# Kernel optimization log

Measured on AMD Instinct MI355X. Metric: run time of the kernel, lower is better.

Reference implementation:

```python
import jax, jax.numpy as jnp
import numpy as np

POOL = 2  # pool_size from init_kwargs


def setup_inputs() -> dict:
    key = jax.random.key(0)
    b, n = 8192, 64
    A = jax.random.normal(key, (b, n, n), dtype=jnp.float32)
    # SPD construction: A A^T / n + I  (well-conditioned, distinct eigvals a.s.)
    X = A @ jnp.swapaxes(A, -1, -2) / n + jnp.eye(n, dtype=jnp.float32)
    return {"X": X}


def _logm_spd(X):
    # matrix log of batched SPD via eigendecomposition (SPDTangentSpace)
    w, V = jnp.linalg.eigh(X)
    return (V * jnp.log(w)[..., None, :]) @ jnp.swapaxes(V, -1, -2)


def _expm_sym(H):
    # matrix exp of batched symmetric matrices (SPDUnTangentSpace)
    w, V = jnp.linalg.eigh(H)
    return (V * jnp.exp(w)[..., None, :]) @ jnp.swapaxes(V, -1, -2)


def reference(X):
    # log map to tangent space
    logX = _logm_spd(X)
    b, n, _ = logX.shape
    m = n // POOL
    # avg_pool2d(kernel=POOL, stride=POOL) over the (n, n) matrix dims
    pooled = logX.reshape(b, m, POOL, m, POOL).mean(axis=(2, 4))
    # pooling of a symmetric matrix with this block pattern stays symmetric;
    # symmetrize for numerical safety before eigh-based exp map
    pooled = 0.5 * (pooled + jnp.swapaxes(pooled, -1, -2))
    return _expm_sym(pooled)
```

## Files before the change

kernel.cpp:

```cpp
#include <hip/hip_runtime.h>

typedef __attribute__((ext_vector_type(8))) short short8;
typedef __attribute__((ext_vector_type(16))) float f32x16;

#define PL 8256
#define SLOT 16448
#define U0O 0
#define U1O SLOT
#define U2O (2 * SLOT)

__device__ __forceinline__ int swadr(int m, int kc) {
  return m * 128 + ((kc ^ (m & 7)) << 4);
}

__device__ __forceinline__ unsigned int cvtpk(float a, float b) {
  unsigned int r;
  asm("v_cvt_pk_bf16_f32 %0, %1, %2" : "=v"(r) : "v"(a), "v"(b));
  return r;
}

__device__ __forceinline__ float dppswap(float v) {
  return __int_as_float(
      __builtin_amdgcn_mov_dpp(__float_as_int(v), 0xB1, 0xF, 0xF, true));
}

__device__ __forceinline__ f32x16 zero16() {
  f32x16 z;
#pragma unroll
  for (int i = 0; i < 16; ++i) z[i] = 0.f;
  return z;
}

__device__ __forceinline__ void q16x16(f32x16& v) {
#pragma unroll
  for (int r = 0; r < 16; r += 2) {
    unsigned w = cvtpk(v[r], v[r + 1]);
    v[r] = __uint_as_float(w << 16);
    v[r + 1] = __uint_as_float(w & 0xFFFF0000u);
  }
}

__device__ __forceinline__ void store_hi8(char* dst, const float* v) {
  uint4 w = make_uint4(cvtpk(v[0], v[1]), cvtpk(v[2], v[3]),
                       cvtpk(v[4], v[5]), cvtpk(v[6], v[7]));
  *(uint4*)dst = w;
}

__device__ __forceinline__ void split_store8(char* dst, const float* v) {
  unsigned h[4], l[4];
#pragma unroll
  for (int j = 0; j < 4; ++j) {
    unsigned hw = cvtpk(v[2 * j], v[2 * j + 1]);
    float h0 = __uint_as_float(hw << 16);
    float h1 = __uint_as_float(hw & 0xFFFF0000u);
    l[j] = cvtpk(v[2 * j] - h0, v[2 * j + 1] - h1);
    h[j] = hw;
  }
  *(uint4*)dst = make_uint4(h[0], h[1], h[2], h[3]);
  *(uint4*)(dst + PL) = make_uint4(l[0], l[1], l[2], l[3]);
}

__device__ __forceinline__ void split_store4(char* dst, const float* v) {
  unsigned h0 = cvtpk(v[0], v[1]), h1 = cvtpk(v[2], v[3]);
  unsigned l0 = cvtpk(v[0] - __uint_as_float(h0 << 16),
                      v[1] - __uint_as_float(h0 & 0xFFFF0000u));
  unsigned l1 = cvtpk(v[2] - __uint_as_float(h1 << 16),
                      v[3] - __uint_as_float(h1 & 0xFFFF0000u));
  *(uint2*)dst = make_uint2(h0, h1);
  *(uint2*)(dst + PL) = make_uint2(l0, l1);
}

template <int NK, int OA, int OB>
__device__ __forceinline__ void mac1(f32x16& acc, char* const (&pA)[4],
                                     char* const (&pB)[4]) {
#pragma unroll
  for (int s = 0; s < NK; ++s) {
    short8 a = *(const short8*)(pA[s] + OA);
    short8 b = *(const short8*)(pB[s] + OB);
    acc = __builtin_amdgcn_mfma_f32_32x32x16_bf16(a, b, acc, 0, 0, 0);
  }
}

template <int NK, int OA, int OB>
__device__ __forceinline__ void mac2A(f32x16& acc, char* const (&pA)[4],
                                      char* const (&pB)[4]) {
#pragma unroll
  for (int s = 0; s < NK; ++s) {
    short8 ah = *(const short8*)(pA[s] + OA);
    short8 al = *(const short8*)(pA[s] + OA + PL);
    short8 b = *(const short8*)(pB[s] + OB);
    acc = __builtin_amdgcn_mfma_f32_32x32x16_bf16(ah, b, acc, 0, 0, 0);
    acc = __builtin_amdgcn_mfma_f32_32x32x16_bf16(al, b, acc, 0, 0, 0);
  }
}

template <int NK, int OA, int OB>
__device__ __forceinline__ void mac2B(f32x16& acc, char* const (&pA)[4],
                                      char* const (&pB)[4]) {
#pragma unroll
  for (int s = 0; s < NK; ++s) {
    short8 a = *(const short8*)(pA[s] + OA);
    short8 bh = *(const short8*)(pB[s] + OB);
    short8 bl = *(const short8*)(pB[s] + OB + PL);
    acc = __builtin_amdgcn_mfma_f32_32x32x16_bf16(a, bh, acc, 0, 0, 0);
    acc = __builtin_amdgcn_mfma_f32_32x32x16_bf16(a, bl, acc, 0, 0, 0);
  }
}

template <int NK, int OA, int OB>
__device__ __forceinline__ void mac3(f32x16& acc, char* const (&pA)[4],
                                     char* const (&pB)[4]) {
#pragma unroll
  for (int s = 0; s < NK; ++s) {
    short8 ah = *(const short8*)(pA[s] + OA);
    short8 al = *(const short8*)(pA[s] + OA + PL);
    short8 bh = *(const short8*)(pB[s] + OB);
    short8 bl = *(const short8*)(pB[s] + OB + PL);
    acc = __builtin_amdgcn_mfma_f32_32x32x16_bf16(ah, bh, acc, 0, 0, 0);
    acc = __builtin_amdgcn_mfma_f32_32x32x16_bf16(ah, bl, acc, 0, 0, 0);
    acc = __builtin_amdgcn_mfma_f32_32x32x16_bf16(al, bh, acc, 0, 0, 0);
  }
}

template <int OFF>
__device__ __forceinline__ void write_hi(char* lds, const int (&wo)[16], bool ev,
                                         const f32x16& vals) {
#pragma unroll
  for (int r = 0; r < 16; ++r) {
    float vn = dppswap(vals[r]);
    unsigned hw = cvtpk(vals[r], vn);
    if (ev) *(unsigned*)(lds + OFF + wo[r]) = hw;
  }
}

template <int OFF>
__device__ __forceinline__ void write_split(char* lds, const int (&wo)[16],
                                            bool ev, int pl, const f32x16& vals,
                                            int r0, int r1) {
#pragma unroll
  for (int r = 0; r < 16; ++r) {
    if (r < r0 || r >= r1) continue;
    float v = vals[r];
    float vn = dppswap(v);
    unsigned hw = cvtpk(v, vn);
    float lo = v - __uint_as_float(hw << 16);
    float lon = dppswap(lo);
    unsigned lw = cvtpk(lon, lo);
    *(unsigned*)(lds + OFF + pl + wo[r]) = ev ? hw : lw;
  }
}

__global__ void __launch_bounds__(256, 3)
spd_pool_kernel(const float* __restrict__ X, float* __restrict__ out) {
  __shared__ __align__(16) char lds[3 * SLOT];

  const int tid = threadIdx.x;
  const int lane = tid & 63;
  const int wv = tid >> 6;
  const int R = (wv >> 1) * 32;
  const int Cc = (wv & 1) * 32;
  const int half = lane >> 5;
  const int ln31 = lane & 31;
  const bool ev = (ln31 & 1) == 0;
  const int pl = ev ? 0 : PL;

  char* pA[4];
  char* pB[4];
#pragma unroll
  for (int s = 0; s < 4; ++s) {
    const int kc = 2 * s + half;
    pA[s] = lds + swadr(R + ln31, kc);
    pB[s] = lds + swadr(Cc + ln31, kc);
  }

  int wo[16];
  {
    const int col0 = Cc + (ln31 & ~1);
    const int cchunk = col0 >> 3, cbyte = (col0 & 7) * 2;
    const int rbase = R + 4 * half;
#pragma unroll
    for (int r = 0; r < 16; ++r) {
      const int m = rbase + (r & 3) + 8 * (r >> 2);
      wo[r] = m * 128 + ((cchunk ^ (m & 7)) << 4) + cbyte;
    }
  }

  f32x16 dmask;
#pragma unroll
  for (int r = 0; r < 16; ++r)
    dmask[r] = (R + (r & 3) + 8 * (r >> 2) + 4 * half == Cc + ln31) ? 1.f : 0.f;

  f32x16 mY, mZ;

  {
    const int em = tid >> 2;
    const int ekc = (tid & 3) * 2;
    const int ec0 = ekc * 8;
    const float ic1 = 1.0f / 6.6f;
    const float* Xg = X + (size_t)blockIdx.x * 4096 + em * 64 + ec0;
    const float4* xp = (const float4*)Xg;
    float4 a = xp[0], b = xp[1], c = xp[2], d = xp[3];
    float v[16] = {a.x * ic1, a.y * ic1, a.z * ic1, a.w * ic1,
                   b.x * ic1, b.y * ic1, b.z * ic1, b.w * ic1,
                   c.x * ic1, c.y * ic1, c.z * ic1, c.w * ic1,
                   d.x * ic1, d.y * ic1, d.z * ic1, d.w * ic1};
    float t[16];
#pragma unroll
    for (int i = 0; i < 16; ++i)
      t[i] = ((em == ec0 + i) ? 1.5f : 0.f) - 0.5f * v[i];
    split_store8(lds + swadr(em, ekc), v);
    split_store8(lds + swadr(em, ekc + 1), v + 8);
    store_hi8(lds + U1O + swadr(em, ekc), t);
    store_hi8(lds + U1O + swadr(em, ekc + 1), t + 8);
  }
  __syncthreads();
  mY = zero16();
  mac1<4, U0O, U1O>(mY, pA, pB);
  write_hi<U2O>(lds, wo, ev, mY);
  __syncthreads();
#pragma unroll 1
  for (int it = 0; it < 4; ++it) {
    f32x16 a;
#pragma unroll
    for (int r = 0; r < 16; ++r) a[r] = -3.f * dmask[r];
    mac1<4, U1O, U2O>(a, pA, pB);
    f32x16 tv;
#pragma unroll
    for (int r = 0; r < 16; ++r) tv[r] = -0.5f * a[r];
    write_hi<U2O + PL>(lds, wo, ev, tv);
    __syncthreads();
    mY = zero16();
    mac1<4, U2O, U2O + PL>(mY, pA, pB);
    mZ = zero16();
    mac1<4, U2O + PL, U1O>(mZ, pA, pB);
    __syncthreads();
    write_hi<U2O>(lds, wo, ev, mY);
    write_hi<U1O>(lds, wo, ev, mZ);
    __syncthreads();
  }
  mY = zero16();
  mac2A<4, U0O, U1O>(mY, pA, pB);
  write_split<U2O>(lds, wo, ev, pl, mY, 0, 16);
  __syncthreads();
  {
    f32x16 a;
#pragma unroll
    for (int r = 0; r < 16; ++r) a[r] = -dmask[r];
    mac2B<4, U1O, U2O>(a, pA, pB);
    f32x16 dv;
#pragma unroll
    for (int r = 0; r < 16; ++r) dv[r] = -0.5f * a[r];
    write_hi<U0O>(lds, wo, ev, dv);
  }
  __syncthreads();
  mac1<4, U2O, U0O>(mY, pA, pB);
  __syncthreads();
  write_split<U2O>(lds, wo, ev, pl, mY, 0, 16);
  {
    f32x16 t0v;
#pragma unroll
    for (int r = 0; r < 16; ++r) t0v[r] = 1.5f * dmask[r] - 0.5f * mY[r];
    write_hi<U1O>(lds, wo, ev, t0v);
  }
  __syncthreads();
  mY = zero16();
  mac1<4, U2O, U1O>(mY, pA, pB);
  write_hi<U0O>(lds, wo, ev, mY);
  __syncthreads();
#pragma unroll 1
  for (int it = 0; it < 2; ++it) {
    f32x16 a;
#pragma unroll
    for (int r = 0; r < 16; ++r) a[r] = -3.f * dmask[r];
    mac1<4, U1O, U0O>(a, pA, pB);
    f32x16 tv;
#pragma unroll
    for (int r = 0; r < 16; ++r) tv[r] = -0.5f * a[r];
    write_hi<U0O + PL>(lds, wo, ev, tv);
    __syncthreads();
    mY = zero16();
    mac1<4, U0O, U0O + PL>(mY, pA, pB);
    mZ = zero16();
    mac1<4, U0O + PL, U1O>(mZ, pA, pB);
    __syncthreads();
    write_hi<U0O>(lds, wo, ev, mY);
    write_hi<U1O>(lds, wo, ev, mZ);
    __syncthreads();
  }
  q16x16(mZ);
  mY = zero16();
  mac2A<4, U2O, U1O>(mY, pA, pB);
  write_split<U0O>(lds, wo, ev, pl, mY, 0, 16);
  __syncthreads();
  {
    f32x16 a;
#pragma unroll
    for (int r = 0; r < 16; ++r) a[r] = -dmask[r];
    mac2B<4, U1O, U0O>(a, pA, pB);
    f32x16 dv;
#pragma unroll
    for (int r = 0; r < 16; ++r) dv[r] = -0.5f * a[r];
    write_hi<U2O>(lds, wo, ev, dv);
  }
  __syncthreads();
  mac1<4, U0O, U2O>(mY, pA, pB);
  mac1<4, U2O, U1O>(mZ, pA, pB);
  __syncthreads();
  write_split<U0O>(lds, wo, ev, pl, mY, 0, 16);
  q16x16(mZ);
  write_hi<U1O>(lds, wo, ev, mZ);
  __syncthreads();
  {
    f32x16 a;
#pragma unroll
    for (int r = 0; r < 16; ++r) a[r] = -dmask[r];
    mac2B<4, U1O, U0O>(a, pA, pB);
    f32x16 dv;
#pragma unroll
    for (int r = 0; r < 16; ++r) dv[r] = -0.5f * a[r];
    write_hi<U2O>(lds, wo, ev, dv);
  }
  __syncthreads();
  mac1<4, U0O, U2O>(mY, pA, pB);
  mac1<4, U2O, U1O>(mZ, pA, pB);
  f32x16 sv;
  {
    const float ca = 0.80141224f;
    const float cb = 0.31194493f;
#pragma unroll
    for (int r = 0; r < 16; ++r) sv[r] = ca * mY[r] - cb * mZ[r];
  }
  __syncthreads();
  write_split<U0O>(lds, wo, ev, pl, sv, 0, 16);
  __syncthreads();
  {
    f32x16 s2 = zero16();
    mac3<4, U0O, U0O>(s2, pA, pB);
    const float A11 = -0.08948864f, A9 = 0.12152778f;
    f32x16 qv;
#pragma unroll
    for (int r = 0; r < 16; ++r) qv[r] = A11 * s2[r] + A9 * dmask[r];
    write_hi<U1O>(lds, wo, ev, s2);
    write_hi<U1O + PL>(lds, wo, ev, qv);
  }
  __syncthreads();
  {
    const float acoef[3] = {-0.17857143f, 0.3f, -0.66666667f};
#pragma unroll 1
    for (int j = 0; j < 3; ++j) {
      f32x16 a;
#pragma unroll
      for (int r = 0; r < 16; ++r) a[r] = acoef[j] * dmask[r];
      mac1<4, U1O + PL, U1O>(a, pA, pB);
      __syncthreads();
      write_hi<U1O + PL>(lds, wo, ev, a);
      __syncthreads();
    }
  }
  {
    f32x16 a;
#pragma unroll
    for (int r = 0; r < 16; ++r) a[r] = 4.f * dmask[r];
    mac1<4, U1O + PL, U1O>(a, pA, pB);
    __syncthreads();
    write_split<U2O>(lds, wo, ev, pl, a, 0, 16);
    __syncthreads();
  }
  {
    f32x16 mL = zero16();
    mac3<4, U0O, U2O>(mL, pA, pB);
    float* Lf = (float*)(lds + U1O);
#pragma unroll
    for (int r = 0; r < 16; ++r)
      Lf[(R + (r & 3) + 8 * (r >> 2) + 4 * half) * 64 + Cc + ln31] = mL[r];
  }
  __syncthreads();
  {
    const float d8 = 2.4801587e-5f, d7 = 1.9841270e-4f;
    const float* Lf = (const float*)(lds + U1O);
    int i = tid >> 3, ct = tid & 7, j4 = ct * 4;
    const float4* r0p = (const float4*)&Lf[(2 * i) * 64 + 8 * ct];
    const float4* r1p = (const float4*)&Lf[(2 * i + 1) * 64 + 8 * ct];
    float4 a0 = r0p[0], a1 = r0p[1], b0 = r1p[0], b1 = r1p[1];
    float p[4], q2v[4];
    p[0] = 0.125f * (a0.x + a0.y + b0.x + b0.y);
    p[1] = 0.125f * (a0.z + a0.w + b0.z + b0.w);
    p[2] = 0.125f * (a1.x + a1.y + b1.x + b1.y);
    p[3] = 0.125f * (a1.z + a1.w + b1.z + b1.w);
#pragma unroll
    for (int qq = 0; qq < 4; ++qq)
      q2v[qq] = d8 * p[qq] + ((i == j4 + qq) ? d7 : 0.f);
    int boff = swadr(i, ct >> 1) + (j4 & 7) * 2;
    split_store4(lds + boff, p);
    split_store4(lds + U2O + boff, q2v);
  }
  __syncthreads();
  char* pE[4];
#pragma unroll
  for (int s = 0; s < 4; ++s) pE[s] = lds + swadr(ln31, 2 * s + half);
  f32x16 dmask2;
#pragma unroll
  for (int r = 0; r < 16; ++r)
    dmask2[r] = ((r & 3) + 8 * (r >> 2) + 4 * half == ln31) ? 1.f : 0.f;
  int wo2[16];
  {
    const int col0 = ln31 & ~1;
    const int cchunk = col0 >> 3, cbyte = (col0 & 7) * 2;
    const int rbase = 4 * half;
#pragma unroll
    for (int r = 0; r < 16; ++r) {
      const int m = rbase + (r & 3) + 8 * (r >> 2);
      wo2[r] = m * 128 + ((cchunk ^ (m & 7)) << 4) + cbyte;
    }
  }
  {
    const float dcoef[7] = {1.f / 720.f, 1.f / 120.f, 1.f / 24.f,
                            1.f / 6.f,   0.5f,        1.f,       1.f};
#pragma unroll 1
    for (int j = 0; j < 7; ++j) {
      f32x16 acc;
#pragma unroll
      for (int r = 0; r < 16; ++r) acc[r] = dcoef[j] * dmask2[r];
      mac3<2, U2O, U0O>(acc, pE, pE);
      __syncthreads();
      write_split<U2O>(lds, wo2, ev, pl, acc, 4 * wv, 4 * wv + 4);
      __syncthreads();
    }
  }
  {
    f32x16 acc = zero16();
    mac3<2, U2O, U2O>(acc, pE, pE);
    float* og = out + (size_t)blockIdx.x * 1024;
#pragma unroll
    for (int r = 0; r < 16; ++r) {
      if (r < 4 * wv || r >= 4 * wv + 4) continue;
      int rl = (r & 3) + 8 * (r >> 2) + 4 * half;
      og[rl * 32 + ln31] = acc[r];
    }
  }
}

extern "C" void kernel_launch(void* const* d_in, const int* in_sizes, int n_in,
                              void* d_out, int out_size, void* d_ws, size_t ws_size,
                              hipStream_t stream) {
  const float* X = (const float*)d_in[0];
  float* out = (float*)d_out;
  const int batch = in_sizes[0] / 4096;
  spd_pool_kernel<<<batch, 256, 0, stream>>>(X, out);
}
```

Baseline: 541.5 us.

## Process each matrix with a single wavefront, removing block barriers

Changes the kernel from four waves per 64x64 matrix, each computing one 32x32 tile, to one 64-lane wave computing all four tiles in registers. This removes every __syncthreads and the cross-wave LDS handoffs, and avg-pooling is now done in registers with DPP instead of through an fp32 LDS staging buffer. LDS is repacked into five 8 KB planes. In exchange each wave does four times the MFMA work serially and holds many more accumulator registers. Per-CU occupancy and latency hiding now depend on how many single-wave blocks can be resident at once.

```diff
diff --git a/kernel.cpp b/kernel.cpp
--- a/kernel.cpp
+++ b/kernel.cpp
@@ -3,35 +3,91 @@
 typedef __attribute__((ext_vector_type(8))) short short8;
 typedef __attribute__((ext_vector_type(16))) float f32x16;
 
-#define PL 8256
-#define SLOT 16448
-#define U0O 0
-#define U1O SLOT
-#define U2O (2 * SLOT)
+#define PP0 0
+#define PP1 8192
+#define PP2 16384
+#define PP3 24576
+#define PP4 32768
+
+#define MFMA32(a, b, c) __builtin_amdgcn_mfma_f32_32x32x16_bf16((a), (b), (c), 0, 0, 0)
 
 __device__ __forceinline__ int swadr(int m, int kc) {
   return m * 128 + ((kc ^ (m & 7)) << 4);
 }
-
-__device__ __forceinline__ unsigned int cvtpk(float a, float b) {
-  unsigned int r;
+__device__ __forceinline__ unsigned cvtpk(float a, float b) {
+  unsigned r;
   asm("v_cvt_pk_bf16_f32 %0, %1, %2" : "=v"(r) : "v"(a), "v"(b));
   return r;
 }
-
 __device__ __forceinline__ float dppswap(float v) {
   return __int_as_float(
       __builtin_amdgcn_mov_dpp(__float_as_int(v), 0xB1, 0xF, 0xF, true));
 }
-
-__device__ __forceinline__ f32x16 zero16() {
-  f32x16 z;
-#pragma unroll
-  for (int i = 0; i < 16; ++i) z[i] = 0.f;
-  return z;
-}
-
-__device__ __forceinline__ void q16x16(f32x16& v) {
+__device__ __forceinline__ short8 ldf(const char* p, int off) {
+  return *(const short8*)(p + off);
+}
+
+template <int OA, int OB, bool SA, bool SB>
+__device__ __forceinline__ void mm64(f32x16& C0, f32x16& C1, f32x16& C2, f32x16& C3,
+                                     const char* lds, const int (&pk)[4]) {
+#pragma unroll
+  for (int s = 0; s < 4; ++s) {
+    short8 a0 = ldf(lds, pk[s] + OA);
+    short8 a1 = ldf(lds, pk[s] + OA + 4096);
+    short8 b0 = ldf(lds, pk[s] + OB);
+    short8 b1 = ldf(lds, pk[s] + OB + 4096);
+    C0 = MFMA32(a0, b0, C0);
+    C1 = MFMA32(a0, b1, C1);
+    C2 = MFMA32(a1, b0, C2);
+    C3 = MFMA32(a1, b1, C3);
+    if constexpr (SB) {
+      short8 b0l = ldf(lds, pk[s] + OB + 8192);
+      short8 b1l = ldf(lds, pk[s] + OB + 8192 + 4096);
+      C0 = MFMA32(a0, b0l, C0);
+      C1 = MFMA32(a0, b1l, C1);
+      C2 = MFMA32(a1, b0l, C2);
+      C3 = MFMA32(a1, b1l, C3);
+    }
+    if constexpr (SA) {
+      short8 a0l = ldf(lds, pk[s] + OA + 8192);
+      short8 a1l = ldf(lds, pk[s] + OA + 8192 + 4096);
+      C0 = MFMA32(a0l, b0, C0);
+      C1 = MFMA32(a0l, b1, C1);
+      C2 = MFMA32(a1l, b0, C2);
+      C3 = MFMA32(a1l, b1, C3);
+    }
+  }
+}
+
+template <int OA, int OB>
+__device__ __forceinline__ void mm32(f32x16& C, const char* lds, const int (&pk)[4]) {
+#pragma unroll
+  for (int s = 0; s < 2; ++s) {
+    short8 ah = ldf(lds, pk[s] + OA);
+    short8 al = ldf(lds, pk[s] + OA + 8192);
+    short8 bh = ldf(lds, pk[s] + OB);
+    short8 bl = ldf(lds, pk[s] + OB + 8192);
+    C = MFMA32(ah, bh, C);
+    C = MFMA32(ah, bl, C);
+    C = MFMA32(al, bh, C);
+  }
+}
+
+__device__ __forceinline__ void z4(f32x16& C0, f32x16& C1, f32x16& C2, f32x16& C3) {
+#pragma unroll
+  for (int r = 0; r < 16; ++r) {
+    C0[r] = 0.f; C1[r] = 0.f; C2[r] = 0.f; C3[r] = 0.f;
+  }
+}
+__device__ __forceinline__ void pre4(f32x16& C0, f32x16& C1, f32x16& C2, f32x16& C3,
+                                     const f32x16& dm, float v) {
+#pragma unroll
+  for (int r = 0; r < 16; ++r) {
+    float d = v * dm[r];
+    C0[r] = d; C3[r] = d; C1[r] = 0.f; C2[r] = 0.f;
+  }
+}
+__device__ __forceinline__ void q16t(f32x16& v) {
 #pragma unroll
   for (int r = 0; r < 16; r += 2) {
     unsigned w = cvtpk(v[r], v[r + 1]);
@@ -40,379 +96,252 @@
   }
 }
 
-__device__ __forceinline__ void store_hi8(char* dst, const float* v) {
-  uint4 w = make_uint4(cvtpk(v[0], v[1]), cvtpk(v[2], v[3]),
-                       cvtpk(v[4], v[5]), cvtpk(v[6], v[7]));
-  *(uint4*)dst = w;
-}
-
-__device__ __forceinline__ void split_store8(char* dst, const float* v) {
-  unsigned h[4], l[4];
-#pragma unroll
-  for (int j = 0; j < 4; ++j) {
-    unsigned hw = cvtpk(v[2 * j], v[2 * j + 1]);
-    float h0 = __uint_as_float(hw << 16);
-    float h1 = __uint_as_float(hw & 0xFFFF0000u);
-    l[j] = cvtpk(v[2 * j] - h0, v[2 * j + 1] - h1);
-    h[j] = hw;
-  }
-  *(uint4*)dst = make_uint4(h[0], h[1], h[2], h[3]);
-  *(uint4*)(dst + PL) = make_uint4(l[0], l[1], l[2], l[3]);
-}
-
-__device__ __forceinline__ void split_store4(char* dst, const float* v) {
-  unsigned h0 = cvtpk(v[0], v[1]), h1 = cvtpk(v[2], v[3]);
-  unsigned l0 = cvtpk(v[0] - __uint_as_float(h0 << 16),
-                      v[1] - __uint_as_float(h0 & 0xFFFF0000u));
-  unsigned l1 = cvtpk(v[2] - __uint_as_float(h1 << 16),
-                      v[3] - __uint_as_float(h1 & 0xFFFF0000u));
-  *(uint2*)dst = make_uint2(h0, h1);
-  *(uint2*)(dst + PL) = make_uint2(l0, l1);
-}
-
-template <int NK, int OA, int OB>
-__device__ __forceinline__ void mac1(f32x16& acc, char* const (&pA)[4],
-                                     char* const (&pB)[4]) {
-#pragma unroll
-  for (int s = 0; s < NK; ++s) {
-    short8 a = *(const short8*)(pA[s] + OA);
-    short8 b = *(const short8*)(pB[s] + OB);
-    acc = __builtin_amdgcn_mfma_f32_32x32x16_bf16(a, b, acc, 0, 0, 0);
-  }
-}
-
-template <int NK, int OA, int OB>
-__device__ __forceinline__ void mac2A(f32x16& acc, char* const (&pA)[4],
-                                      char* const (&pB)[4]) {
-#pragma unroll
-  for (int s = 0; s < NK; ++s) {
-    short8 ah = *(const short8*)(pA[s] + OA);
-    short8 al = *(const short8*)(pA[s] + OA + PL);
-    short8 b = *(const short8*)(pB[s] + OB);
-    acc = __builtin_amdgcn_mfma_f32_32x32x16_bf16(ah, b, acc, 0, 0, 0);
-    acc = __builtin_amdgcn_mfma_f32_32x32x16_bf16(al, b, acc, 0, 0, 0);
-  }
-}
-
-template <int NK, int OA, int OB>
-__device__ __forceinline__ void mac2B(f32x16& acc, char* const (&pA)[4],
-                                      char* const (&pB)[4]) {
-#pragma unroll
-  for (int s = 0; s < NK; ++s) {
-    short8 a = *(const short8*)(pA[s] + OA);
-    short8 bh = *(const short8*)(pB[s] + OB);
-    short8 bl = *(const short8*)(pB[s] + OB + PL);
-    acc = __builtin_amdgcn_mfma_f32_32x32x16_bf16(a, bh, acc, 0, 0, 0);
-    acc = __builtin_amdgcn_mfma_f32_32x32x16_bf16(a, bl, acc, 0, 0, 0);
-  }
-}
-
-template <int NK, int OA, int OB>
-__device__ __forceinline__ void mac3(f32x16& acc, char* const (&pA)[4],
-                                     char* const (&pB)[4]) {
-#pragma unroll
-  for (int s = 0; s < NK; ++s) {
-    short8 ah = *(const short8*)(pA[s] + OA);
-    short8 al = *(const short8*)(pA[s] + OA + PL);
-    short8 bh = *(const short8*)(pB[s] + OB);
-    short8 bl = *(const short8*)(pB[s] + OB + PL);
-    acc = __builtin_amdgcn_mfma_f32_32x32x16_bf16(ah, bh, acc, 0, 0, 0);
-    acc = __builtin_amdgcn_mfma_f32_32x32x16_bf16(ah, bl, acc, 0, 0, 0);
-    acc = __builtin_amdgcn_mfma_f32_32x32x16_bf16(al, bh, acc, 0, 0, 0);
+template <int OFF, bool SCALE, bool ADDI>
+__device__ __forceinline__ void wrhi64(char* lds, const int (&wo)[16], bool ev, int jd,
+                                       const f32x16& C0, const f32x16& C1,
+                                       const f32x16& C2, const f32x16& C3,
+                                       const f32x16& dm, float al, float be) {
+#pragma unroll
+  for (int t = 0; t < 4; ++t) {
+    const f32x16& C = t == 0 ? C0 : t == 1 ? C1 : t == 2 ? C2 : C3;
+    const int base = OFF + (t >> 1) * 4096 + ((t & 1) ? jd : 0);
+#pragma unroll
+    for (int r = 0; r < 16; ++r) {
+      float v = SCALE ? al * C[r] : C[r];
+      if (ADDI && (t == 0 || t == 3)) v += be * dm[r];
+      float vn = dppswap(v);
+      unsigned hw = cvtpk(v, vn);
+      if (ev) *(unsigned*)(lds + base + wo[r]) = hw;
+    }
   }
 }
 
 template <int OFF>
-__device__ __forceinline__ void write_hi(char* lds, const int (&wo)[16], bool ev,
-                                         const f32x16& vals) {
+__device__ __forceinline__ void wrsp64(char* lds, const int (&wo)[16], bool ev, int pl,
+                                       int jd, const f32x16& C0, const f32x16& C1,
+                                       const f32x16& C2, const f32x16& C3) {
+#pragma unroll
+  for (int t = 0; t < 4; ++t) {
+    const f32x16& C = t == 0 ? C0 : t == 1 ? C1 : t == 2 ? C2 : C3;
+    const int base = OFF + (t >> 1) * 4096 + ((t & 1) ? jd : 0) + pl;
+#pragma unroll
+    for (int r = 0; r < 16; ++r) {
+      float v = C[r];
+      float vn = dppswap(v);
+      unsigned hw = cvtpk(v, vn);
+      float lo = v - __uint_as_float(hw << 16);
+      float lon = dppswap(lo);
+      unsigned lw = cvtpk(lon, lo);
+      *(unsigned*)(lds + base + wo[r]) = ev ? hw : lw;
+    }
+  }
+}
+
+template <int OFF>
+__device__ __forceinline__ void wrsp32(char* lds, const int (&wo)[16], bool ev, int pl,
+                                       const f32x16& C) {
+  const int base = OFF + pl;
 #pragma unroll
   for (int r = 0; r < 16; ++r) {
-    float vn = dppswap(vals[r]);
-    unsigned hw = cvtpk(vals[r], vn);
-    if (ev) *(unsigned*)(lds + OFF + wo[r]) = hw;
-  }
-}
-
-template <int OFF>
-__device__ __forceinline__ void write_split(char* lds, const int (&wo)[16],
-                                            bool ev, int pl, const f32x16& vals,
-                                            int r0, int r1) {
-#pragma unroll
-  for (int r = 0; r < 16; ++r) {
-    if (r < r0 || r >= r1) continue;
-    float v = vals[r];
+    float v = C[r];
     float vn = dppswap(v);
     unsigned hw = cvtpk(v, vn);
     float lo = v - __uint_as_float(hw << 16);
     float lon = dppswap(lo);
     unsigned lw = cvtpk(lon, lo);
-    *(unsigned*)(lds + OFF + pl + wo[r]) = ev ? hw : lw;
-  }
-}
-
-__global__ void __launch_bounds__(256, 3)
+    *(unsigned*)(lds + base + wo[r]) = ev ? hw : lw;
+  }
+}
+
+__global__ void __launch_bounds__(64, 1)
 spd_pool_kernel(const float* __restrict__ X, float* __restrict__ out) {
-  __shared__ __align__(16) char lds[3 * SLOT];
-
-  const int tid = threadIdx.x;
-  const int lane = tid & 63;
-  const int wv = tid >> 6;
-  const int R = (wv >> 1) * 32;
-  const int Cc = (wv & 1) * 32;
+  __shared__ __align__(16) char lds[40960];
+
+  const int lane = threadIdx.x;
   const int half = lane >> 5;
   const int ln31 = lane & 31;
   const bool ev = (ln31 & 1) == 0;
-  const int pl = ev ? 0 : PL;
-
-  char* pA[4];
-  char* pB[4];
-#pragma unroll
-  for (int s = 0; s < 4; ++s) {
-    const int kc = 2 * s + half;
-    pA[s] = lds + swadr(R + ln31, kc);
-    pB[s] = lds + swadr(Cc + ln31, kc);
-  }
+  const int pl = ev ? 0 : 8192;
+  const int jd = half ? -64 : 64;
+
+  int pk[4];
+#pragma unroll
+  for (int s = 0; s < 4; ++s) pk[s] = swadr(ln31, 2 * s + half);
 
   int wo[16];
   {
-    const int col0 = Cc + (ln31 & ~1);
+    const int col0 = ln31 & ~1;
     const int cchunk = col0 >> 3, cbyte = (col0 & 7) * 2;
-    const int rbase = R + 4 * half;
+    const int rb = 4 * half;
 #pragma unroll
     for (int r = 0; r < 16; ++r) {
-      const int m = rbase + (r & 3) + 8 * (r >> 2);
+      const int m = rb + (r & 3) + 8 * (r >> 2);
       wo[r] = m * 128 + ((cchunk ^ (m & 7)) << 4) + cbyte;
     }
   }
-
   f32x16 dmask;
 #pragma unroll
   for (int r = 0; r < 16; ++r)
-    dmask[r] = (R + (r & 3) + 8 * (r >> 2) + 4 * half == Cc + ln31) ? 1.f : 0.f;
-
-  f32x16 mY, mZ;
-
-  {
-    const int em = tid >> 2;
-    const int ekc = (tid & 3) * 2;
-    const int ec0 = ekc * 8;
+    dmask[r] = ((r & 3) + 8 * (r >> 2) + 4 * half == ln31) ? 1.f : 0.f;
+
+  {
     const float ic1 = 1.0f / 6.6f;
-    const float* Xg = X + (size_t)blockIdx.x * 4096 + em * 64 + ec0;
-    const float4* xp = (const float4*)Xg;
-    float4 a = xp[0], b = xp[1], c = xp[2], d = xp[3];
-    float v[16] = {a.x * ic1, a.y * ic1, a.z * ic1, a.w * ic1,
-                   b.x * ic1, b.y * ic1, b.z * ic1, b.w * ic1,
-                   c.x * ic1, c.y * ic1, c.z * ic1, c.w * ic1,
-                   d.x * ic1, d.y * ic1, d.z * ic1, d.w * ic1};
-    float t[16];
-#pragma unroll
-    for (int i = 0; i < 16; ++i)
-      t[i] = ((em == ec0 + i) ? 1.5f : 0.f) - 0.5f * v[i];
-    split_store8(lds + swadr(em, ekc), v);
-    split_store8(lds + swadr(em, ekc + 1), v + 8);
-    store_hi8(lds + U1O + swadr(em, ekc), t);
-    store_hi8(lds + U1O + swadr(em, ekc + 1), t + 8);
-  }
-  __syncthreads();
-  mY = zero16();
-  mac1<4, U0O, U1O>(mY, pA, pB);
-  write_hi<U2O>(lds, wo, ev, mY);
-  __syncthreads();
+    const float* Xg = X + (size_t)blockIdx.x * 4096;
+    const int rr = lane >> 4;
+    const int c0 = (lane & 15) * 4;
+    const int kc = c0 >> 3;
+    const int sub = (lane & 1) * 8;
+#pragma unroll
+    for (int k = 0; k < 16; ++k) {
+      const int row = 4 * k + rr;
+      float4 x = *(const float4*)(Xg + row * 64 + c0);
+      float v0 = x.x * ic1, v1 = x.y * ic1, v2 = x.z * ic1, v3 = x.w * ic1;
+      unsigned h0 = cvtpk(v0, v1), h1 = cvtpk(v2, v3);
+      unsigned l0 = cvtpk(v0 - __uint_as_float(h0 << 16),
+                          v1 - __uint_as_float(h0 & 0xFFFF0000u));
+      unsigned l1 = cvtpk(v2 - __uint_as_float(h1 << 16),
+                          v3 - __uint_as_float(h1 & 0xFFFF0000u));
+      float t0 = ((row == c0) ? 1.5f : 0.f) - 0.5f * v0;
+      float t1 = ((row == c0 + 1) ? 1.5f : 0.f) - 0.5f * v1;
+      float t2 = ((row == c0 + 2) ? 1.5f : 0.f) - 0.5f * v2;
+      float t3 = ((row == c0 + 3) ? 1.5f : 0.f) - 0.5f * v3;
+      unsigned s0 = cvtpk(t0, t1), s1 = cvtpk(t2, t3);
+      const int off = swadr(row, kc) + sub;
+      *(uint2*)(lds + PP0 + off) = make_uint2(h0, h1);
+      *(uint2*)(lds + PP1 + off) = make_uint2(l0, l1);
+      *(uint2*)(lds + PP2 + off) = make_uint2(s0, s1);
+    }
+  }
+
+  f32x16 Y0, Y1, Y2, Y3, Z0, Z1, Z2, Z3, A0, A1, A2, A3;
+
+  z4(Y0, Y1, Y2, Y3);
+  mm64<PP0, PP2, false, false>(Y0, Y1, Y2, Y3, lds, pk);
+  wrhi64<PP3, false, false>(lds, wo, ev, jd, Y0, Y1, Y2, Y3, dmask, 0.f, 0.f);
+
 #pragma unroll 1
   for (int it = 0; it < 4; ++it) {
-    f32x16 a;
-#pragma unroll
-    for (int r = 0; r < 16; ++r) a[r] = -3.f * dmask[r];
-    mac1<4, U1O, U2O>(a, pA, pB);
-    f32x16 tv;
-#pragma unroll
-    for (int r = 0; r < 16; ++r) tv[r] = -0.5f * a[r];
-    write_hi<U2O + PL>(lds, wo, ev, tv);
-    __syncthreads();
-    mY = zero16();
-    mac1<4, U2O, U2O + PL>(mY, pA, pB);
-    mZ = zero16();
-    mac1<4, U2O + PL, U1O>(mZ, pA, pB);
-    __syncthreads();
-    write_hi<U2O>(lds, wo, ev, mY);
-    write_hi<U1O>(lds, wo, ev, mZ);
-    __syncthreads();
-  }
-  mY = zero16();
-  mac2A<4, U0O, U1O>(mY, pA, pB);
-  write_split<U2O>(lds, wo, ev, pl, mY, 0, 16);
-  __syncthreads();
-  {
-    f32x16 a;
-#pragma unroll
-    for (int r = 0; r < 16; ++r) a[r] = -dmask[r];
-    mac2B<4, U1O, U2O>(a, pA, pB);
-    f32x16 dv;
-#pragma unroll
-    for (int r = 0; r < 16; ++r) dv[r] = -0.5f * a[r];
-    write_hi<U0O>(lds, wo, ev, dv);
-  }
-  __syncthreads();
-  mac1<4, U2O, U0O>(mY, pA, pB);
-  __syncthreads();
-  write_split<U2O>(lds, wo, ev, pl, mY, 0, 16);
-  {
-    f32x16 t0v;
-#pragma unroll
-    for (int r = 0; r < 16; ++r) t0v[r] = 1.5f * dmask[r] - 0.5f * mY[r];
-    write_hi<U1O>(lds, wo, ev, t0v);
-  }
-  __syncthreads();
-  mY = zero16();
-  mac1<4, U2O, U1O>(mY, pA, pB);
-  write_hi<U0O>(lds, wo, ev, mY);
-  __syncthreads();
+    pre4(A0, A1, A2, A3, dmask, -3.f);
+    mm64<PP2, PP3, false, false>(A0, A1, A2, A3, lds, pk);
+    wrhi64<PP4, true, false>(lds, wo, ev, jd, A0, A1, A2, A3, dmask, -0.5f, 0.f);
+    z4(Y0, Y1, Y2, Y3);
+    mm64<PP3, PP4, false, false>(Y0, Y1, Y2, Y3, lds, pk);
+    z4(Z0, Z1, Z2, Z3);
+    mm64<PP4, PP2, false, false>(Z0, Z1, Z2, Z3, lds, pk);
+    wrhi64<PP3, false, false>(lds, wo, ev, jd, Y0, Y1, Y2, Y3, dmask, 0.f, 0.f);
+    wrhi64<PP2, false, false>(lds, wo, ev, jd, Z0, Z1, Z2, Z3, dmask, 0.f, 0.f);
+  }
+
+  z4(Y0, Y1, Y2, Y3);
+  mm64<PP0, PP2, true, false>(Y0, Y1, Y2, Y3, lds, pk);
+  wrsp64<PP3>(lds, wo, ev, pl, jd, Y0, Y1, Y2, Y3);
+  pre4(A0, A1, A2, A3, dmask, -1.f);
+  mm64<PP2, PP3, false, true>(A0, A1, A2, A3, lds, pk);
+  wrhi64<PP0, true, false>(lds, wo, ev, jd, A0, A1, A2, A3, dmask, -0.5f, 0.f);
+  mm64<PP3, PP0, false, false>(Y0, Y1, Y2, Y3, lds, pk);
+  wrsp64<PP3>(lds, wo, ev, pl, jd, Y0, Y1, Y2, Y3);
+  wrhi64<PP2, true, true>(lds, wo, ev, jd, Y0, Y1, Y2, Y3, dmask, -0.5f, 1.5f);
+
+  z4(A0, A1, A2, A3);
+  mm64<PP3, PP2, false, false>(A0, A1, A2, A3, lds, pk);
+  wrhi64<PP0, false, false>(lds, wo, ev, jd, A0, A1, A2, A3, dmask, 0.f, 0.f);
+
 #pragma unroll 1
   for (int it = 0; it < 2; ++it) {
-    f32x16 a;
-#pragma unroll
-    for (int r = 0; r < 16; ++r) a[r] = -3.f * dmask[r];
-    mac1<4, U1O, U0O>(a, pA, pB);
-    f32x16 tv;
-#pragma unroll
-    for (int r = 0; r < 16; ++r) tv[r] = -0.5f * a[r];
-    write_hi<U0O + PL>(lds, wo, ev, tv);
-    __syncthreads();
-    mY = zero16();
-    mac1<4, U0O, U0O + PL>(mY, pA, pB);
-    mZ = zero16();
-    mac1<4, U0O + PL, U1O>(mZ, pA, pB);
-    __syncthreads();
-    write_hi<U0O>(lds, wo, ev, mY);
-    write_hi<U1O>(lds, wo, ev, mZ);
-    __syncthreads();
-  }
-  q16x16(mZ);
-  mY = zero16();
-  mac2A<4, U2O, U1O>(mY, pA, pB);
-  write_split<U0O>(lds, wo, ev, pl, mY, 0, 16);
-  __syncthreads();
-  {
-    f32x16 a;
-#pragma unroll
-    for (int r = 0; r < 16; ++r) a[r] = -dmask[r];
-    mac2B<4, U1O, U0O>(a, pA, pB);
-    f32x16 dv;
-#pragma unroll
-    for (int r = 0; r < 16; ++r) dv[r] = -0.5f * a[r];
-    write_hi<U2O>(lds, wo, ev, dv);
-  }
-  __syncthreads();
-  mac1<4, U0O, U2O>(mY, pA, pB);
-  mac1<4, U2O, U1O>(mZ, pA, pB);
-  __syncthreads();
-  write_split<U0O>(lds, wo, ev, pl, mY, 0, 16);
-  q16x16(mZ);
-  write_hi<U1O>(lds, wo, ev, mZ);
-  __syncthreads();
-  {
-    f32x16 a;
-#pragma unroll
-    for (int r = 0; r < 16; ++r) a[r] = -dmask[r];
-    mac2B<4, U1O, U0O>(a, pA, pB);
-    f32x16 dv;
-#pragma unroll
-    for (int r = 0; r < 16; ++r) dv[r] = -0.5f * a[r];
-    write_hi<U2O>(lds, wo, ev, dv);
-  }
-  __syncthreads();
-  mac1<4, U0O, U2O>(mY, pA, pB);
-  mac1<4, U2O, U1O>(mZ, pA, pB);
-  f32x16 sv;
+    pre4(A0, A1, A2, A3, dmask, -3.f);
+    mm64<PP2, PP0, false, false>(A0, A1, A2, A3, lds, pk);
+    wrhi64<PP1, true, false>(lds, wo, ev, jd, A0, A1, A2, A3, dmask, -0.5f, 0.f);
+    z4(Y0, Y1, Y2, Y3);
+    mm64<PP0, PP1, false, false>(Y0, Y1, Y2, Y3, lds, pk);
+    z4(Z0, Z1, Z2, Z3);
+    mm64<PP1, PP2, false, false>(Z0, Z1, Z2, Z3, lds, pk);
+    wrhi64<PP0, false, false>(lds, wo, ev, jd, Y0, Y1, Y2, Y3, dmask, 0.f, 0.f);
+    wrhi64<PP2, false, false>(lds, wo, ev, jd, Z0, Z1, Z2, Z3, dmask, 0.f, 0.f);
+  }
+
+  q16t(Z0); q16t(Z1); q16t(Z2); q16t(Z3);
+  z4(Y0, Y1, Y2, Y3);
+  mm64<PP3, PP2, true, false>(Y0, Y1, Y2, Y3, lds, pk);
+  wrsp64<PP0>(lds, wo, ev, pl, jd, Y0, Y1, Y2, Y3);
+  pre4(A0, A1, A2, A3, dmask, -1.f);
+  mm64<PP2, PP0, false, true>(A0, A1, A2, A3, lds, pk);
+  wrhi64<PP3, true, false>(lds, wo, ev, jd, A0, A1, A2, A3, dmask, -0.5f, 0.f);
+  mm64<PP0, PP3, false, false>(Y0, Y1, Y2, Y3, lds, pk);
+  mm64<PP3, PP2, false, false>(Z0, Z1, Z2, Z3, lds, pk);
+  wrsp64<PP0>(lds, wo, ev, pl, jd, Y0, Y1, Y2, Y3);
+  q16t(Z0); q16t(Z1); q16t(Z2); q16t(Z3);
+  wrhi64<PP2, false, false>(lds, wo, ev, jd, Z0, Z1, Z2, Z3, dmask, 0.f, 0.f);
+  pre4(A0, A1, A2, A3, dmask, -1.f);
+  mm64<PP2, PP0, false, true>(A0, A1, A2, A3, lds, pk);
+  wrhi64<PP3, true, false>(lds, wo, ev, jd, A0, A1, A2, A3, dmask, -0.5f, 0.f);
+  mm64<PP0, PP3, false, false>(Y0, Y1, Y2, Y3, lds, pk);
+  mm64<PP3, PP2, false, false>(Z0, Z1, Z2, Z3, lds, pk);
+
   {
     const float ca = 0.80141224f;
     const float cb = 0.31194493f;
 #pragma unroll
-    for (int r = 0; r < 16; ++r) sv[r] = ca * mY[r] - cb * mZ[r];
-  }
-  __syncthreads();
-  write_split<U0O>(lds, wo, ev, pl, sv, 0, 16);
-  __syncthreads();
-  {
-    f32x16 s2 = zero16();
-    mac3<4, U0O, U0O>(s2, pA, pB);
-    const float A11 = -0.08948864f, A9 = 0.12152778f;
-    f32x16 qv;
-#pragma unroll
-    for (int r = 0; r < 16; ++r) qv[r] = A11 * s2[r] + A9 * dmask[r];
-    write_hi<U1O>(lds, wo, ev, s2);
-    write_hi<U1O + PL>(lds, wo, ev, qv);
-  }
-  __syncthreads();
+    for (int r = 0; r < 16; ++r) {
+      A0[r] = ca * Y0[r] - cb * Z0[r];
+      A1[r] = ca * Y1[r] - cb * Z1[r];
+      A2[r] = ca * Y2[r] - cb * Z2[r];
+      A3[r] = ca * Y3[r] - cb * Z3[r];
+    }
+  }
+  wrsp64<PP0>(lds, wo, ev, pl, jd, A0, A1, A2, A3);
+
+  z4(Y0, Y1, Y2, Y3);
+  mm64<PP0, PP0, true, true>(Y0, Y1, Y2, Y3, lds, pk);
+  wrhi64<PP2, false, false>(lds, wo, ev, jd, Y0, Y1, Y2, Y3, dmask, 0.f, 0.f);
+  wrhi64<PP3, true, true>(lds, wo, ev, jd, Y0, Y1, Y2, Y3, dmask, -0.08948864f,
+                          0.12152778f);
+
   {
     const float acoef[3] = {-0.17857143f, 0.3f, -0.66666667f};
 #pragma unroll 1
     for (int j = 0; j < 3; ++j) {
-      f32x16 a;
-#pragma unroll
-      for (int r = 0; r < 16; ++r) a[r] = acoef[j] * dmask[r];
-      mac1<4, U1O + PL, U1O>(a, pA, pB);
-      __syncthreads();
-      write_hi<U1O + PL>(lds, wo, ev, a);
-      __syncthreads();
-    }
-  }
-  {
-    f32x16 a;
-#pragma unroll
-    for (int r = 0; r < 16; ++r) a[r] = 4.f * dmask[r];
-    mac1<4, U1O + PL, U1O>(a, pA, pB);
-    __syncthreads();
-    write_split<U2O>(lds, wo, ev, pl, a, 0, 16);
-    __syncthreads();
-  }
-  {
-    f32x16 mL = zero16();
-    mac3<4, U0O, U2O>(mL, pA, pB);
-    float* Lf = (float*)(lds + U1O);
-#pragma unroll
-    for (int r = 0; r < 16; ++r)
-      Lf[(R + (r & 3) + 8 * (r >> 2) + 4 * half) * 64 + Cc + ln31] = mL[r];
-  }
-  __syncthreads();
+      pre4(A0, A1, A2, A3, dmask, acoef[j]);
+      mm64<PP3, PP2, false, false>(A0, A1, A2, A3, lds, pk);
+      wrhi64<PP3, false, false>(lds, wo, ev, jd, A0, A1, A2, A3, dmask, 0.f, 0.f);
+    }
+  }
+  pre4(A0, A1, A2, A3, dmask, 4.f);
+  mm64<PP3, PP2, false, false>(A0, A1, A2, A3, lds, pk);
+  wrsp64<PP3>(lds, wo, ev, pl, jd, A0, A1, A2, A3);
+
+  z4(Y0, Y1, Y2, Y3);
+  mm64<PP0, PP3, true, true>(Y0, Y1, Y2, Y3, lds, pk);
   {
     const float d8 = 2.4801587e-5f, d7 = 1.9841270e-4f;
-    const float* Lf = (const float*)(lds + U1O);
-    int i = tid >> 3, ct = tid & 7, j4 = ct * 4;
-    const float4* r0p = (const float4*)&Lf[(2 * i) * 64 + 8 * ct];
-    const float4* r1p = (const float4*)&Lf[(2 * i + 1) * 64 + 8 * ct];
-    float4 a0 = r0p[0], a1 = r0p[1], b0 = r1p[0], b1 = r1p[1];
-    float p[4], q2v[4];
-    p[0] = 0.125f * (a0.x + a0.y + b0.x + b0.y);
-    p[1] = 0.125f * (a0.z + a0.w + b0.z + b0.w);
-    p[2] = 0.125f * (a1.x + a1.y + b1.x + b1.y);
-    p[3] = 0.125f * (a1.z + a1.w + b1.z + b1.w);
-#pragma unroll
-    for (int qq = 0; qq < 4; ++qq)
-      q2v[qq] = d8 * p[qq] + ((i == j4 + qq) ? d7 : 0.f);
-    int boff = swadr(i, ct >> 1) + (j4 & 7) * 2;
-    split_store4(lds + boff, p);
-    split_store4(lds + U2O + boff, q2v);
-  }
-  __syncthreads();
-  char* pE[4];
-#pragma unroll
-  for (int s = 0; s < 4; ++s) pE[s] = lds + swadr(ln31, 2 * s + half);
-  f32x16 dmask2;
-#pragma unroll
-  for (int r = 0; r < 16; ++r)
-    dmask2[r] = ((r & 3) + 8 * (r >> 2) + 4 * half == ln31) ? 1.f : 0.f;
-  int wo2[16];
-  {
-    const int col0 = ln31 & ~1;
-    const int cchunk = col0 >> 3, cbyte = (col0 & 7) * 2;
-    const int rbase = 4 * half;
-#pragma unroll
-    for (int r = 0; r < 16; ++r) {
-      const int m = rbase + (r & 3) + 8 * (r >> 2);
-      wo2[r] = m * 128 + ((cchunk ^ (m & 7)) << 4) + cbyte;
-    }
-  }
+#pragma unroll
+    for (int t = 0; t < 4; ++t) {
+      const f32x16& C = t == 0 ? Y0 : t == 1 ? Y1 : t == 2 ? Y2 : Y3;
+      const int bi = (t >> 1) * 16, bj = (t & 1) * 16;
+#pragma unroll
+      for (int q = 0; q < 8; ++q) {
+        float rp = C[2 * q] + C[2 * q + 1];
+        float cs = rp + dppswap(rp);
+        float p = 0.125f * cs;
+        const int row = bi + (q & 1) + 4 * (q >> 1) + 2 * half;
+        const int col = bj + (ln31 >> 1);
+        float qv = d8 * p + ((row == col) ? d7 : 0.f);
+        unsigned phw = cvtpk(p, p);
+        float plo = p - __uint_as_float(phw << 16);
+        unsigned plw = cvtpk(plo, plo);
+        unsigned qhw = cvtpk(qv, qv);
+        float qlo = qv - __uint_as_float(qhw << 16);
+        unsigned qlw = cvtpk(qlo, qlo);
+        const int off = row * 128 + (((col >> 3) ^ (row & 7)) << 4) + (col & 7) * 2;
+        if (ev) {
+          *(short*)(lds + PP0 + off) = (short)phw;
+          *(short*)(lds + PP1 + off) = (short)plw;
+          *(short*)(lds + PP2 + off) = (short)qhw;
+          *(short*)(lds + PP3 + off) = (short)qlw;
+        }
+      }
+    }
+  }
+
   {
     const float dcoef[7] = {1.f / 720.f, 1.f / 120.f, 1.f / 24.f,
                             1.f / 6.f,   0.5f,        1.f,       1.f};
@@ -420,23 +349,21 @@
     for (int j = 0; j < 7; ++j) {
       f32x16 acc;
 #pragma unroll
-      for (int r = 0; r < 16; ++r) acc[r] = dcoef[j] * dmask2[r];
-      mac3<2, U2O, U0O>(acc, pE, pE);
-      __syncthreads();
-      write_split<U2O>(lds, wo2, ev, pl, acc, 4 * wv, 4 * wv + 4);
-      __syncthreads();
-    }
-  }
-  {
-    f32x16 acc = zero16();
-    mac3<2, U2O, U2O>(acc, pE, pE);
+      for (int r = 0; r < 16; ++r) acc[r] = dcoef[j] * dmask[r];
+      mm32<PP2, PP0>(acc, lds, pk);
+      wrsp32<PP2>(lds, wo, ev, pl, acc);
+    }
+  }
+
+  {
+    f32x16 acc;
+#pragma unroll
+    for (int r = 0; r < 16; ++r) acc[r] = 0.f;
+    mm32<PP2, PP2>(acc, lds, pk);
     float* og = out + (size_t)blockIdx.x * 1024;
 #pragma unroll
-    for (int r = 0; r < 16; ++r) {
-      if (r < 4 * wv || r >= 4 * wv + 4) continue;
-      int rl = (r & 3) + 8 * (r >> 2) + 4 * half;
-      og[rl * 32 + ln31] = acc[r];
-    }
+    for (int r = 0; r < 16; ++r)
+      og[((r & 3) + 8 * (r >> 2) + 4 * half) * 32 + ln31] = acc[r];
   }
 }
 
@@ -446,5 +373,5 @@
   const float* X = (const float*)d_in[0];
   float* out = (float*)d_out;
   const int batch = in_sizes[0] / 4096;
-  spd_pool_kernel<<<batch, 256, 0, stream>>>(X, out);
-}
+  spd_pool_kernel<<<batch, 64, 0, stream>>>(X, out);
+}
```

Result: slower. 684.4 us (+26.4%).
